# Performance work log

Hardware: AMD Instinct MI355X
Metric: run time of the kernel (lower is better)

Reference implementation:

```python
import jax, jax.numpy as jnp
import numpy as np

R = 32       # voxel_resolution
GROUPS = 8   # GroupNorm groups
EPS = 1e-5


def setup_inputs() -> dict:
    key = jax.random.key(0)
    ks = jax.random.split(key, 8)
    B, N, Cin, Cout = 4, 16384, 64, 128
    coords = jax.random.uniform(ks[0], (B, N, 3), dtype=jnp.float32)
    features = jax.random.normal(ks[1], (B, Cin, N), dtype=jnp.float32) * 0.5
    s1 = 1.0 / np.sqrt(Cin * 27)
    s2 = 1.0 / np.sqrt(Cout * 27)
    sm = 1.0 / np.sqrt(Cin)
    return {
        "coords": coords,
        "features": features,
        "conv1_w": jax.random.normal(ks[2], (Cout, Cin, 3, 3, 3), dtype=jnp.float32) * s1,
        "conv1_b": jnp.zeros((Cout,), jnp.float32),
        "gn1_g": jnp.ones((Cout,), jnp.float32),
        "gn1_b": jnp.zeros((Cout,), jnp.float32),
        "conv2_w": jax.random.normal(ks[3], (Cout, Cout, 3, 3, 3), dtype=jnp.float32) * s2,
        "conv2_b": jnp.zeros((Cout,), jnp.float32),
        "gn2_g": jnp.ones((Cout,), jnp.float32),
        "gn2_b": jnp.zeros((Cout,), jnp.float32),
        "mlp_w": jax.random.normal(ks[4], (Cout, Cin), dtype=jnp.float32) * sm,
        "mlp_b": jnp.zeros((Cout,), jnp.float32),
        "gnp_g": jnp.ones((Cout,), jnp.float32),
        "gnp_b": jnp.zeros((Cout,), jnp.float32),
    }


def _group_norm(x, gamma, beta, axes):
    # x: [B, C, ...]; normalize within channel groups over `axes` of the
    # grouped view [B, G, C//G, ...]. axes=(2,) => per-location GN (matches
    # nn.GroupNorm applied to per-voxel feature rows [Nvox, C]).
    B, C = x.shape[0], x.shape[1]
    xr = x.reshape(B, GROUPS, C // GROUPS, *x.shape[2:])
    mu = xr.mean(axis=axes, keepdims=True)
    var = ((xr - mu) ** 2).mean(axis=axes, keepdims=True)
    xn = ((xr - mu) * jax.lax.rsqrt(var + EPS)).reshape(x.shape)
    shp = (1, C) + (1,) * (x.ndim - 2)
    return xn * gamma.reshape(shp) + beta.reshape(shp)


def _conv3(x, w, b):
    y = jax.lax.conv_general_dilated(
        x, w, (1, 1, 1), 'SAME',
        dimension_numbers=('NCDHW', 'OIDHW', 'NCDHW'))
    return y + b.reshape(1, -1, 1, 1, 1)


def reference(coords, features, conv1_w, conv1_b, gn1_g, gn1_b,
              conv2_w, conv2_b, gn2_g, gn2_b, mlp_w, mlp_b, gnp_g, gnp_b):
    B, Cin, N = features.shape
    Cout = conv1_w.shape[0]

    # ---- voxelize: average-scatter point features into [B,Cin,R,R,R] ----
    c = coords * R                               # voxel-unit coords in [0,R)
    lo = jnp.floor(c)
    idx = jnp.clip(lo.astype(jnp.int32), 0, R - 1)   # [B,N,3]
    bidx = jnp.arange(B, dtype=jnp.int32)[:, None]
    flat = ((bidx * R + idx[..., 0]) * R + idx[..., 1]) * R + idx[..., 2]
    seg = flat.reshape(-1)                       # [B*N]
    fT = features.transpose(0, 2, 1).reshape(B * N, Cin)
    sums = jax.ops.segment_sum(fT, seg, num_segments=B * R * R * R)
    cnt = jax.ops.segment_sum(jnp.ones((B * N,), fT.dtype), seg,
                              num_segments=B * R * R * R)
    grid = (sums / jnp.maximum(cnt, 1.0)[:, None]).reshape(
        B, R, R, R, Cin).transpose(0, 4, 1, 2, 3)

    # ---- voxel branch: conv -> GN -> SiLU -> (dropout=id) -> conv -> GN -> SiLU
    h = jax.nn.silu(_group_norm(_conv3(grid, conv1_w, conv1_b), gn1_g, gn1_b, (2,)))
    h = jax.nn.silu(_group_norm(_conv3(h, conv2_w, conv2_b), gn2_g, gn2_b, (2,)))

    # ---- trilinear devoxelize: gather-interpolate back to points ----
    frac = c - lo                                # [B,N,3]
    hi = jnp.clip(idx + 1, 0, R - 1)
    gridf = h.transpose(0, 2, 3, 4, 1).reshape(B, R * R * R, Cout)
    barange = jnp.arange(B)[:, None]
    out = jnp.zeros((B, N, Cout), h.dtype)
    for dx in (0, 1):
        wx = frac[..., 0] if dx else 1.0 - frac[..., 0]
        ix = hi[..., 0] if dx else idx[..., 0]
        for dy in (0, 1):
            wy = frac[..., 1] if dy else 1.0 - frac[..., 1]
            iy = hi[..., 1] if dy else idx[..., 1]
            for dz in (0, 1):
                wz = frac[..., 2] if dz else 1.0 - frac[..., 2]
                iz = hi[..., 2] if dz else idx[..., 2]
                fi = (ix * R + iy) * R + iz       # [B,N]
                vals = gridf[barange, fi]         # [B,N,Cout]
                out = out + (wx * wy * wz)[..., None] * vals
    vox_pts = out.transpose(0, 2, 1)              # [B,Cout,N]

    # ---- point branch: SharedMLP = 1x1 conv + GroupNorm + SiLU ----
    pf = jnp.einsum('oi,bin->bon', mlp_w, features) + mlp_b[None, :, None]
    pf = jax.nn.silu(_group_norm(pf, gnp_g, gnp_b, (2, 3)))

    return pf + vox_pts
```

## Files before the change

### kernel.cpp

```cpp
#include <hip/hip_runtime.h>

typedef unsigned short u16;
typedef __attribute__((ext_vector_type(8))) short s16x8;
typedef __attribute__((ext_vector_type(4))) float f32x4;

#define R3 32768
#define NPTS 16384

__device__ __forceinline__ float b2f(u16 u) {
  union { unsigned int i; float f; } v; v.i = ((unsigned int)u) << 16; return v.f;
}
__device__ __forceinline__ u16 f2b(float f) {
  union { float f; unsigned int i; } v; v.f = f;
  unsigned int x = v.i;
  return (u16)((x + 0x7fffu + ((x >> 16) & 1u)) >> 16);
}
__device__ __forceinline__ void split2(float x, u16& h, u16& l) {
  h = f2b(x); l = f2b(x - b2f(h));
}
__device__ __forceinline__ float silu(float x) {
  return x / (1.f + __expf(-x));
}

__global__ void convert_weights(const float* __restrict__ w1, const float* __restrict__ w2,
                                const float* __restrict__ wm,
                                u16* __restrict__ Wh1, u16* __restrict__ Wl1,
                                u16* __restrict__ Wh2, u16* __restrict__ Wl2,
                                u16* __restrict__ Whm, u16* __restrict__ Wlm) {
  int e = blockIdx.x * 256 + threadIdx.x;
  if (e < 27 * 128 * 64) {
    int t = e / (128 * 64), co = (e / 64) % 128, ci = e % 64;
    split2(w1[(co * 64 + ci) * 27 + t], Wh1[e], Wl1[e]);
  }
  if (e < 27 * 128 * 128) {
    int t = e / (128 * 128), co = (e / 128) % 128, ci = e % 128;
    split2(w2[(co * 128 + ci) * 27 + t], Wh2[e], Wl2[e]);
  }
  if (e < 128 * 64) split2(wm[e], Whm[e], Wlm[e]);
}

__global__ void __launch_bounds__(256)
scatter_feats(const float* __restrict__ coords, const float* __restrict__ features,
              float* __restrict__ Gsum, float* __restrict__ Gcnt) {
  __shared__ float trans[64][65];
  __shared__ int vox[64];
  const int tid = threadIdx.x;
  const int bi = blockIdx.x >> 8;
  const int n0 = (blockIdx.x & 255) << 6;
  if (tid < 64) {
    const float* cp = coords + ((size_t)bi * NPTS + n0 + tid) * 3;
    int ix = min(max((int)floorf(cp[0] * 32.f), 0), 31);
    int iy = min(max((int)floorf(cp[1] * 32.f), 0), 31);
    int iz = min(max((int)floorf(cp[2] * 32.f), 0), 31);
    vox[tid] = (ix * 32 + iy) * 32 + iz;
  }
  for (int e = tid; e < 4096; e += 256) {
    int ci = e >> 6, nn = e & 63;
    trans[nn][ci] = features[((size_t)bi * 64 + ci) * NPTS + n0 + nn];
  }
  __syncthreads();
  const int wave = tid >> 6, lane = tid & 63;
  for (int pi = 0; pi < 16; ++pi) {
    int nn = wave * 16 + pi;
    int v = vox[nn];
    atomicAdd(&Gsum[((size_t)bi * R3 + v) * 64 + lane], trans[nn][lane]);
    if (lane == 0) atomicAdd(&Gcnt[bi * R3 + v], 1.f);
  }
}

__global__ void __launch_bounds__(256)
finalize_grid(const float* __restrict__ Gsum, const float* __restrict__ Gcnt,
              u16* __restrict__ X1) {
  size_t g = (size_t)blockIdx.x * 256 + threadIdx.x;
  float c = fmaxf(Gcnt[g >> 4], 1.f);
  float4 s = ((const float4*)Gsum)[g];
  unsigned h0 = f2b(s.x / c), h1 = f2b(s.y / c), h2 = f2b(s.z / c), h3 = f2b(s.w / c);
  uint2 o; o.x = h0 | (h1 << 16); o.y = h2 | (h3 << 16);
  *(uint2*)(X1 + g * 4) = o;
}

template<int CIN>
__global__ void __launch_bounds__(128, 2)
conv_mfma_w2(const u16* __restrict__ X, const u16* __restrict__ Wh, const u16* __restrict__ Wl,
             const float* __restrict__ bias, const float* __restrict__ gamma,
             const float* __restrict__ beta, u16* __restrict__ Yb) {
  constexpr int CINP = CIN + 8;
  constexpr int ROWS = 136;
  constexpr int KS = CIN / 32;
  constexpr int CH8 = CIN / 8;
  constexpr int XBYTES = ROWS * CINP * 2;
  constexpr int OBYTES = 128 * 136 * 2;
  constexpr int LBYTES = (XBYTES > OBYTES) ? XBYTES : OBYTES;
  __shared__ __align__(16) char ldsbuf[LBYTES];
  u16* Xs = (u16*)ldsbuf;
  u16* Os = (u16*)ldsbuf;

  const int tid = threadIdx.x;
  const int wave = tid >> 6, lane = tid & 63;
  const int l15 = lane & 15, q = lane >> 4;
  const int co0 = wave * 64;

  const int bi = blockIdx.x >> 8;
  const int rem = blockIdx.x & 255;
  const int x = rem >> 3, y0 = (rem & 7) << 2;

  u16 oneb = f2b(1.0f), lidb = f2b((float)(l15 + 1));
  s16x8 vone, vlid;
#pragma unroll
  for (int e = 0; e < 8; ++e) { vone[e] = (short)oneb; vlid[e] = (short)lidb; }
  f32x4 z4 = {0.f, 0.f, 0.f, 0.f};
  f32x4 d1 = __builtin_amdgcn_mfma_f32_16x16x32_bf16(vlid, vone, z4, 0, 0, 0);
  f32x4 d2 = __builtin_amdgcn_mfma_f32_16x16x32_bf16(vone, vlid, z4, 0, 0, 0);
  int mdec[4], ndec[4];
#pragma unroll
  for (int r = 0; r < 4; ++r) {
    mdec[r] = (int)(d1[r] * 0.03125f + 0.5f) - 1;
    ndec[r] = (int)(d2[r] * 0.03125f + 0.5f) - 1;
  }

  f32x4 acc[4][8];
#pragma unroll
  for (int a = 0; a < 4; ++a)
#pragma unroll
    for (int b = 0; b < 8; ++b) acc[a][b] = (f32x4){0.f, 0.f, 0.f, 0.f};

  for (int g = 0; g < 9; ++g) {
    __syncthreads();
    const int dx = g / 3 - 1, dy = g % 3 - 1;
    const int xs = x + dx;
    for (int c = tid; c < ROWS * CH8; c += 128) {
      int rr = c / CH8, k = (c % CH8) * 8;
      uint4 val; val.x = val.y = val.z = val.w = 0u;
      int vy = rr / 34;
      int zz = rr - vy * 34 - 1;
      int ys = y0 + vy + dy;
      if (xs >= 0 && xs < 32 && ys >= 0 && ys < 32 && zz >= 0 && zz < 32)
        val = *(const uint4*)(X + ((size_t)bi * R3 + (size_t)((xs * 32 + ys) * 32 + zz)) * CIN + k);
      *(uint4*)(&Xs[rr * CINP + k]) = val;
    }
    __syncthreads();
    for (int dz = 0; dz < 3; ++dz) {
      const int t = g * 3 + dz;
#pragma unroll
      for (int kb = 0; kb < KS; ++kb) {
        const int ko = kb * 32 + q * 8;
        s16x8 ah[4], al[4], bb[8];
#pragma unroll
        for (int ct = 0; ct < 4; ++ct) {
          size_t wo = ((size_t)(t * 128 + co0 + ct * 16 + l15)) * CIN + ko;
          ah[ct] = *(const s16x8*)(Wh + wo);
          al[ct] = *(const s16x8*)(Wl + wo);
        }
#pragma unroll
        for (int vt = 0; vt < 8; ++vt)
          bb[vt] = *(const s16x8*)(
              &Xs[((vt >> 1) * 34 + (vt & 1) * 16 + l15 + dz) * CINP + ko]);
#pragma unroll
        for (int ct = 0; ct < 4; ++ct)
#pragma unroll
          for (int vt = 0; vt < 8; ++vt) {
            acc[ct][vt] = __builtin_amdgcn_mfma_f32_16x16x32_bf16(
                ah[ct], bb[vt], acc[ct][vt], 0, 0, 0);
            acc[ct][vt] = __builtin_amdgcn_mfma_f32_16x16x32_bf16(
                al[ct], bb[vt], acc[ct][vt], 0, 0, 0);
          }
      }
    }
  }

  __syncthreads();
#pragma unroll
  for (int ct = 0; ct < 4; ++ct) {
    float bi4[4], g4[4], be4[4];
#pragma unroll
    for (int r = 0; r < 4; ++r) {
      int coL = co0 + ct * 16 + mdec[r];
      bi4[r] = bias[coL]; g4[r] = gamma[coL]; be4[r] = beta[coL];
    }
#pragma unroll
    for (int vt = 0; vt < 8; ++vt) {
      float v[4];
#pragma unroll
      for (int r = 0; r < 4; ++r) v[r] = acc[ct][vt][r] + bi4[r];
      float s = v[0] + v[1] + v[2] + v[3];
      s += __shfl_xor(s, 16); s += __shfl_xor(s, 32);
      float mu = s * 0.0625f;
      float qv = 0.f;
#pragma unroll
      for (int r = 0; r < 4; ++r) { float d = v[r] - mu; qv = fmaf(d, d, qv); }
      qv += __shfl_xor(qv, 16); qv += __shfl_xor(qv, 32);
      float rs = rsqrtf(qv * 0.0625f + 1e-5f);
      int vox = vt * 16 + l15;
#pragma unroll
      for (int r = 0; r < 4; ++r) {
        float xn = (v[r] - mu) * rs * g4[r] + be4[r];
        Os[vox * 136 + co0 + ct * 16 + mdec[r]] = f2b(silu(xn));
      }
    }
  }
  __syncthreads();
  for (int e = tid; e < 2048; e += 128) {
    int vox = e >> 4, c8 = (e & 15) * 8;
    int yl = vox >> 5, z = vox & 31;
    size_t row = (size_t)bi * R3 + (size_t)((x * 32 + y0 + yl) * 32 + z);
    *(uint4*)(Yb + row * 128 + c8) = *(const uint4*)(&Os[vox * 136 + c8]);
  }
}

__global__ void __launch_bounds__(256)
mlp_mfma(const float* __restrict__ features, const u16* __restrict__ Whm,
         const u16* __restrict__ Wlm, const float* __restrict__ mb,
         u16* __restrict__ pf, float* __restrict__ stats) {
  constexpr int XBYTES = 64 * 72 * 2;
  constexpr int SBYTES = 4 * 64 * 33 * 4;
  __shared__ __align__(16) char ldsbuf[(XBYTES > SBYTES) ? XBYTES : SBYTES];
  u16* Xs = (u16*)ldsbuf;
  float* ldsW = (float*)ldsbuf;

  const int tid = threadIdx.x;
  const int wave = tid >> 6, lane = tid & 63;
  const int l15 = lane & 15, q = lane >> 4;
  const int cobase = wave * 32;
  const int bi = blockIdx.x >> 8;
  const int n0 = (blockIdx.x & 255) << 6;

  u16 oneb = f2b(1.0f), lidb = f2b((float)(l15 + 1));
  s16x8 vone, vlid;
#pragma unroll
  for (int e = 0; e < 8; ++e) { vone[e] = (short)oneb; vlid[e] = (short)lidb; }
  f32x4 z4 = {0.f, 0.f, 0.f, 0.f};
  f32x4 d1 = __builtin_amdgcn_mfma_f32_16x16x32_bf16(vlid, vone, z4, 0, 0, 0);
  f32x4 d2 = __builtin_amdgcn_mfma_f32_16x16x32_bf16(vone, vlid, z4, 0, 0, 0);
  int mdec[4], ndec[4];
#pragma unroll
  for (int r = 0; r < 4; ++r) {
    mdec[r] = (int)(d1[r] * 0.03125f + 0.5f) - 1;
    ndec[r] = (int)(d2[r] * 0.03125f + 0.5f) - 1;
  }

  for (int e = tid; e < 4096; e += 256) {
    int ci = e >> 6, nn = e & 63;
    Xs[nn * 72 + ci] = f2b(features[((size_t)bi * 64 + ci) * NPTS + n0 + nn]);
  }
  __syncthreads();

  f32x4 acc[2][4];
#pragma unroll
  for (int a = 0; a < 2; ++a)
#pragma unroll
    for (int b = 0; b < 4; ++b) acc[a][b] = (f32x4){0.f, 0.f, 0.f, 0.f};

#pragma unroll
  for (int kb = 0; kb < 2; ++kb) {
    const int ko = kb * 32 + q * 8;
    s16x8 ah[2], al[2], bb[4];
#pragma unroll
    for (int ct = 0; ct < 2; ++ct) {
      size_t wo = ((size_t)(cobase + ct * 16 + l15)) * 64 + ko;
      ah[ct] = *(const s16x8*)(Whm + wo);
      al[ct] = *(const s16x8*)(Wlm + wo);
    }
#pragma unroll
    for (int vt = 0; vt < 4; ++vt)
      bb[vt] = *(const s16x8*)(&Xs[(vt * 16 + l15) * 72 + ko]);
#pragma unroll
    for (int ct = 0; ct < 2; ++ct)
#pragma unroll
      for (int vt = 0; vt < 4; ++vt) {
        acc[ct][vt] = __builtin_amdgcn_mfma_f32_16x16x32_bf16(ah[ct], bb[vt], acc[ct][vt], 0, 0, 0);
        acc[ct][vt] = __builtin_amdgcn_mfma_f32_16x16x32_bf16(al[ct], bb[vt], acc[ct][vt], 0, 0, 0);
      }
  }

  __syncthreads();
#pragma unroll
  for (int ct = 0; ct < 2; ++ct)
#pragma unroll
    for (int vt = 0; vt < 4; ++vt)
#pragma unroll
      for (int r = 0; r < 4; ++r)
        ldsW[(wave * 64 + vt * 16 + ndec[r]) * 33 + ct * 16 + mdec[r]] = acc[ct][vt][r];
  __syncthreads();

  float v[32];
  float s0 = 0.f, q0 = 0.f, s1 = 0.f, q1 = 0.f;
#pragma unroll
  for (int j = 0; j < 32; ++j) {
    v[j] = ldsW[(wave * 64 + lane) * 33 + j] + mb[cobase + j];
    if (j < 16) { s0 += v[j]; q0 = fmaf(v[j], v[j], q0); }
    else        { s1 += v[j]; q1 = fmaf(v[j], v[j], q1); }
  }
  u16 outv[32];
#pragma unroll
  for (int j = 0; j < 32; ++j) outv[j] = f2b(v[j]);
  u16* yp = pf + ((size_t)bi * NPTS + n0 + lane) * 128 + cobase;
#pragma unroll
  for (int k = 0; k < 4; ++k) *(uint4*)(yp + 8 * k) = *(uint4*)(outv + 8 * k);

#pragma unroll
  for (int off = 32; off > 0; off >>= 1) {
    s0 += __shfl_xor(s0, off); q0 += __shfl_xor(q0, off);
    s1 += __shfl_xor(s1, off); q1 += __shfl_xor(q1, off);
  }
  if (lane == 0) {
    atomicAdd(&stats[(bi * 8 + 2 * wave + 0) * 2 + 0], s0);
    atomicAdd(&stats[(bi * 8 + 2 * wave + 0) * 2 + 1], q0);
    atomicAdd(&stats[(bi * 8 + 2 * wave + 1) * 2 + 0], s1);
    atomicAdd(&stats[(bi * 8 + 2 * wave + 1) * 2 + 1], q1);
  }
}

__global__ void __launch_bounds__(256)
final_fuse(const float* __restrict__ coords, const u16* __restrict__ H,
           const u16* __restrict__ pf, const float* __restrict__ stats,
           const float* __restrict__ gg, const float* __restrict__ gb,
           float* __restrict__ out) {
  __shared__ float trans[64][130];
  const int tid = threadIdx.x;
  const int wave = tid >> 6, lane = tid & 63;
  const int bi = blockIdx.x >> 8;
  const int p0 = (blockIdx.x & 255) << 6;
  const int co = lane * 2;
  const int grp = co >> 4;
  const float cntInv = 1.f / (16.f * 16384.f);
  float S  = stats[(bi * 8 + grp) * 2 + 0];
  float SS = stats[(bi * 8 + grp) * 2 + 1];
  float mu = S * cntInv;
  float var = SS * cntInv - mu * mu;
  float rs = rsqrtf(var + 1e-5f);
  float g0 = gg[co], g1 = gg[co + 1], b0 = gb[co], b1 = gb[co + 1];

  for (int pi = 0; pi < 16; ++pi) {
    int pl = wave * 16 + pi;
    int p = p0 + pl;
    const float* cp = coords + ((size_t)bi * NPTS + p) * 3;
    float cx = cp[0] * 32.f, cy = cp[1] * 32.f, cz = cp[2] * 32.f;
    float fx = floorf(cx), fy = floorf(cy), fz = floorf(cz);
    int ix = min(max((int)fx, 0), 31);
    int iy = min(max((int)fy, 0), 31);
    int iz = min(max((int)fz, 0), 31);
    float rx = cx - fx, ry = cy - fy, rz = cz - fz;
    int hx = min(ix + 1, 31), hy = min(iy + 1, 31), hz = min(iz + 1, 31);
    float a0 = 0.f, a1 = 0.f;
#pragma unroll
    for (int k = 0; k < 8; ++k) {
      int xb = k >> 2, yb = (k >> 1) & 1, zb = k & 1;
      float w = (xb ? rx : 1.f - rx) * (yb ? ry : 1.f - ry) * (zb ? rz : 1.f - rz);
      int vi = ((xb ? hx : ix) * 32 + (yb ? hy : iy)) * 32 + (zb ? hz : iz);
      unsigned hv = *(const unsigned*)(H + ((size_t)bi * R3 + vi) * 128 + co);
      a0 += w * b2f((u16)(hv & 0xffff));
      a1 += w * b2f((u16)(hv >> 16));
    }
    unsigned pv = *(const unsigned*)(pf + ((size_t)bi * NPTS + p) * 128 + co);
    float q0 = (b2f((u16)(pv & 0xffff)) - mu) * rs * g0 + b0;
    float q1 = (b2f((u16)(pv >> 16)) - mu) * rs * g1 + b1;
    trans[pl][co]     = silu(q0) + a0;
    trans[pl][co + 1] = silu(q1) + a1;
  }
  __syncthreads();
  for (int e = tid; e < 8192; e += 256) {
    int c = e >> 6, pp = e & 63;
    out[((size_t)bi * 128 + c) * NPTS + p0 + pp] = trans[pp][c];
  }
}

extern "C" void kernel_launch(void* const* d_in, const int* in_sizes, int n_in,
                              void* d_out, int out_size, void* d_ws, size_t ws_size,
                              hipStream_t stream) {
  const float* coords   = (const float*)d_in[0];
  const float* features = (const float*)d_in[1];
  const float* conv1_w  = (const float*)d_in[2];
  const float* conv1_b  = (const float*)d_in[3];
  const float* gn1_g    = (const float*)d_in[4];
  const float* gn1_b    = (const float*)d_in[5];
  const float* conv2_w  = (const float*)d_in[6];
  const float* conv2_b  = (const float*)d_in[7];
  const float* gn2_g    = (const float*)d_in[8];
  const float* gn2_b    = (const float*)d_in[9];
  const float* mlp_w    = (const float*)d_in[10];
  const float* mlp_b    = (const float*)d_in[11];
  const float* gnp_g    = (const float*)d_in[12];
  const float* gnp_b    = (const float*)d_in[13];

  char* ws = (char*)d_ws;
  float* Gsum = (float*)(ws + 0);
  u16*   H    = (u16*)(ws + 0);
  u16*   X1   = (u16*)(ws + 33554432);
  u16*   X2   = (u16*)(ws + 50331648);
  float* Gcnt = (float*)(ws + 83886080);
  float* stats = (float*)(ws + 84410368);
  u16*   pf   = (u16*)(ws + 84676608);
  u16*   Wh1  = (u16*)(ws + 101453824);
  u16*   Wl1  = (u16*)(ws + 101896192);
  u16*   Wh2  = (u16*)(ws + 102338560);
  u16*   Wl2  = (u16*)(ws + 103223296);
  u16*   Whm  = (u16*)(ws + 104108032);
  u16*   Wlm  = (u16*)(ws + 104124416);

  hipMemsetAsync(ws, 0, 33554432, stream);
  hipMemsetAsync(ws + 83886080, 0, 524288 + 4096, stream);

  convert_weights<<<(27 * 128 * 128 + 255) / 256, 256, 0, stream>>>(
      conv1_w, conv2_w, mlp_w, Wh1, Wl1, Wh2, Wl2, Whm, Wlm);
  scatter_feats<<<1024, 256, 0, stream>>>(coords, features, Gsum, Gcnt);
  finalize_grid<<<8192, 256, 0, stream>>>(Gsum, Gcnt, X1);
  conv_mfma_w2<64><<<1024, 128, 0, stream>>>(
      X1, Wh1, Wl1, conv1_b, gn1_g, gn1_b, X2);
  mlp_mfma<<<1024, 256, 0, stream>>>(features, Whm, Wlm, mlp_b, pf, stats);
  conv_mfma_w2<128><<<1024, 128, 0, stream>>>(
      X2, Wh2, Wl2, conv2_b, gn2_g, gn2_b, H);
  final_fuse<<<1024, 256, 0, stream>>>(coords, H, pf, stats, gnp_g, gnp_b,
                                       (float*)d_out);
}
```

Before: 673.0 us.

## Restructure 3D conv to 32x32 MFMA tiles with 4 waves and x-slab staging

The conv kernel now uses 32x32x16 bf16 MFMA instead of 16x16x32 and runs 4 waves per block instead of 2. Waves split output channels in halves and voxel rows in pairs. The LDS tile now holds a 6x34 y/z slab per x offset, so only 3 staging passes and barrier pairs are needed instead of 9, and the dy shifts are taken by indexing inside LDS. The GroupNorm epilogue is rewritten for the 32x32 accumulator layout, with two groups per tile. In exchange the kernel uses more LDS per block, makes more weight loads per MFMA, and drops the occupancy hint from launch bounds.

```diff
diff --git a/kernel.cpp b/kernel.cpp
--- a/kernel.cpp
+++ b/kernel.cpp
@@ -3,6 +3,7 @@
 typedef unsigned short u16;
 typedef __attribute__((ext_vector_type(8))) short s16x8;
 typedef __attribute__((ext_vector_type(4))) float f32x4;
+typedef __attribute__((ext_vector_type(16))) float f32x16;
 
 #define R3 32768
 #define NPTS 16384
@@ -80,14 +81,15 @@
 }
 
 template<int CIN>
-__global__ void __launch_bounds__(128, 2)
-conv_mfma_w2(const u16* __restrict__ X, const u16* __restrict__ Wh, const u16* __restrict__ Wl,
-             const float* __restrict__ bias, const float* __restrict__ gamma,
-             const float* __restrict__ beta, u16* __restrict__ Yb) {
+__global__ void __launch_bounds__(256)
+conv_mfma_s32(const u16* __restrict__ X, const u16* __restrict__ Wh, const u16* __restrict__ Wl,
+              const float* __restrict__ bias, const float* __restrict__ gamma,
+              const float* __restrict__ beta, u16* __restrict__ Yb) {
   constexpr int CINP = CIN + 8;
-  constexpr int ROWS = 136;
-  constexpr int KS = CIN / 32;
+  constexpr int ROWS = 204;
   constexpr int CH8 = CIN / 8;
+  constexpr int NCH = ROWS * CH8;
+  constexpr int NSI = CIN / 16;
   constexpr int XBYTES = ROWS * CINP * 2;
   constexpr int OBYTES = 128 * 136 * 2;
   constexpr int LBYTES = (XBYTES > OBYTES) ? XBYTES : OBYTES;
@@ -97,109 +99,124 @@
 
   const int tid = threadIdx.x;
   const int wave = tid >> 6, lane = tid & 63;
-  const int l15 = lane & 15, q = lane >> 4;
-  const int co0 = wave * 64;
+  const int l31 = lane & 31, kh = lane >> 5;
+  const int cohalf = wave & 1, vh = wave >> 1;
+  const int co0 = cohalf * 64;
 
   const int bi = blockIdx.x >> 8;
   const int rem = blockIdx.x & 255;
   const int x = rem >> 3, y0 = (rem & 7) << 2;
 
-  u16 oneb = f2b(1.0f), lidb = f2b((float)(l15 + 1));
+  u16 oneb = f2b(1.0f), lidb = f2b((float)(l31 + 1));
   s16x8 vone, vlid;
 #pragma unroll
   for (int e = 0; e < 8; ++e) { vone[e] = (short)oneb; vlid[e] = (short)lidb; }
-  f32x4 z4 = {0.f, 0.f, 0.f, 0.f};
-  f32x4 d1 = __builtin_amdgcn_mfma_f32_16x16x32_bf16(vlid, vone, z4, 0, 0, 0);
-  f32x4 d2 = __builtin_amdgcn_mfma_f32_16x16x32_bf16(vone, vlid, z4, 0, 0, 0);
-  int mdec[4], ndec[4];
-#pragma unroll
-  for (int r = 0; r < 4; ++r) {
-    mdec[r] = (int)(d1[r] * 0.03125f + 0.5f) - 1;
-    ndec[r] = (int)(d2[r] * 0.03125f + 0.5f) - 1;
-  }
-
-  f32x4 acc[4][8];
-#pragma unroll
-  for (int a = 0; a < 4; ++a)
-#pragma unroll
-    for (int b = 0; b < 8; ++b) acc[a][b] = (f32x4){0.f, 0.f, 0.f, 0.f};
-
-  for (int g = 0; g < 9; ++g) {
+  f32x16 z16;
+#pragma unroll
+  for (int r = 0; r < 16; ++r) z16[r] = 0.f;
+  f32x16 d1 = __builtin_amdgcn_mfma_f32_32x32x16_bf16(vlid, vone, z16, 0, 0, 0);
+  int mdec[16];
+#pragma unroll
+  for (int r = 0; r < 16; ++r)
+    mdec[r] = (int)(d1[r] * 0.0625f + 0.5f) - 1;
+
+  f32x16 acc[2][2];
+#pragma unroll
+  for (int a = 0; a < 2; ++a)
+#pragma unroll
+    for (int b = 0; b < 2; ++b)
+#pragma unroll
+      for (int r = 0; r < 16; ++r) acc[a][b][r] = 0.f;
+
+  for (int dxs = 0; dxs < 3; ++dxs) {
     __syncthreads();
-    const int dx = g / 3 - 1, dy = g % 3 - 1;
-    const int xs = x + dx;
-    for (int c = tid; c < ROWS * CH8; c += 128) {
+    const int xs = x + dxs - 1;
+    for (int c = tid; c < NCH; c += 256) {
       int rr = c / CH8, k = (c % CH8) * 8;
       uint4 val; val.x = val.y = val.z = val.w = 0u;
-      int vy = rr / 34;
-      int zz = rr - vy * 34 - 1;
-      int ys = y0 + vy + dy;
+      int jy = rr / 34;
+      int pz = rr - jy * 34;
+      int ys = y0 + jy - 1, zz = pz - 1;
       if (xs >= 0 && xs < 32 && ys >= 0 && ys < 32 && zz >= 0 && zz < 32)
         val = *(const uint4*)(X + ((size_t)bi * R3 + (size_t)((xs * 32 + ys) * 32 + zz)) * CIN + k);
       *(uint4*)(&Xs[rr * CINP + k]) = val;
     }
     __syncthreads();
-    for (int dz = 0; dz < 3; ++dz) {
-      const int t = g * 3 + dz;
-#pragma unroll
-      for (int kb = 0; kb < KS; ++kb) {
-        const int ko = kb * 32 + q * 8;
-        s16x8 ah[4], al[4], bb[8];
-#pragma unroll
-        for (int ct = 0; ct < 4; ++ct) {
-          size_t wo = ((size_t)(t * 128 + co0 + ct * 16 + l15)) * CIN + ko;
-          ah[ct] = *(const s16x8*)(Wh + wo);
-          al[ct] = *(const s16x8*)(Wl + wo);
+    for (int dy = 0; dy < 3; ++dy) {
+      const int tb = dxs * 9 + dy * 3;
+#pragma unroll
+      for (int dz = 0; dz < 3; ++dz) {
+        const int t = tb + dz;
+#pragma unroll
+        for (int si = 0; si < NSI; ++si) {
+          const int ko = si * 16 + kh * 8;
+          s16x8 ah[2], al[2], bb[2];
+#pragma unroll
+          for (int ct = 0; ct < 2; ++ct) {
+            size_t wo = ((size_t)(t * 128 + co0 + ct * 32 + l31)) * CIN + ko;
+            ah[ct] = *(const s16x8*)(Wh + wo);
+            al[ct] = *(const s16x8*)(Wl + wo);
+          }
+#pragma unroll
+          for (int vt = 0; vt < 2; ++vt)
+            bb[vt] = *(const s16x8*)(
+                &Xs[((dy + vh * 2 + vt) * 34 + l31 + dz) * CINP + ko]);
+#pragma unroll
+          for (int ct = 0; ct < 2; ++ct)
+#pragma unroll
+            for (int vt = 0; vt < 2; ++vt) {
+              acc[ct][vt] = __builtin_amdgcn_mfma_f32_32x32x16_bf16(
+                  ah[ct], bb[vt], acc[ct][vt], 0, 0, 0);
+              acc[ct][vt] = __builtin_amdgcn_mfma_f32_32x32x16_bf16(
+                  al[ct], bb[vt], acc[ct][vt], 0, 0, 0);
+            }
         }
-#pragma unroll
-        for (int vt = 0; vt < 8; ++vt)
-          bb[vt] = *(const s16x8*)(
-              &Xs[((vt >> 1) * 34 + (vt & 1) * 16 + l15 + dz) * CINP + ko]);
-#pragma unroll
-        for (int ct = 0; ct < 4; ++ct)
-#pragma unroll
-          for (int vt = 0; vt < 8; ++vt) {
-            acc[ct][vt] = __builtin_amdgcn_mfma_f32_16x16x32_bf16(
-                ah[ct], bb[vt], acc[ct][vt], 0, 0, 0);
-            acc[ct][vt] = __builtin_amdgcn_mfma_f32_16x16x32_bf16(
-                al[ct], bb[vt], acc[ct][vt], 0, 0, 0);
-          }
       }
     }
   }
 
   __syncthreads();
 #pragma unroll
-  for (int ct = 0; ct < 4; ++ct) {
-    float bi4[4], g4[4], be4[4];
-#pragma unroll
-    for (int r = 0; r < 4; ++r) {
-      int coL = co0 + ct * 16 + mdec[r];
-      bi4[r] = bias[coL]; g4[r] = gamma[coL]; be4[r] = beta[coL];
-    }
-#pragma unroll
-    for (int vt = 0; vt < 8; ++vt) {
-      float v[4];
-#pragma unroll
-      for (int r = 0; r < 4; ++r) v[r] = acc[ct][vt][r] + bi4[r];
-      float s = v[0] + v[1] + v[2] + v[3];
-      s += __shfl_xor(s, 16); s += __shfl_xor(s, 32);
-      float mu = s * 0.0625f;
-      float qv = 0.f;
-#pragma unroll
-      for (int r = 0; r < 4; ++r) { float d = v[r] - mu; qv = fmaf(d, d, qv); }
-      qv += __shfl_xor(qv, 16); qv += __shfl_xor(qv, 32);
-      float rs = rsqrtf(qv * 0.0625f + 1e-5f);
-      int vox = vt * 16 + l15;
-#pragma unroll
-      for (int r = 0; r < 4; ++r) {
-        float xn = (v[r] - mu) * rs * g4[r] + be4[r];
-        Os[vox * 136 + co0 + ct * 16 + mdec[r]] = f2b(silu(xn));
+  for (int ct = 0; ct < 2; ++ct) {
+    float bi16[16], g16[16], be16[16];
+#pragma unroll
+    for (int r = 0; r < 16; ++r) {
+      int coL = co0 + ct * 32 + mdec[r];
+      bi16[r] = bias[coL]; g16[r] = gamma[coL]; be16[r] = beta[coL];
+    }
+#pragma unroll
+    for (int vt = 0; vt < 2; ++vt) {
+      float vv[16];
+      float s0 = 0.f, s1 = 0.f;
+#pragma unroll
+      for (int r = 0; r < 16; ++r) {
+        vv[r] = acc[ct][vt][r] + bi16[r];
+        if (mdec[r] < 16) s0 += vv[r]; else s1 += vv[r];
       }
-    }
-  }
-  __syncthreads();
-  for (int e = tid; e < 2048; e += 128) {
+      s0 += __shfl_xor(s0, 32); s1 += __shfl_xor(s1, 32);
+      float mu0 = s0 * 0.0625f, mu1 = s1 * 0.0625f;
+      float q0 = 0.f, q1 = 0.f;
+#pragma unroll
+      for (int r = 0; r < 16; ++r) {
+        float mu = (mdec[r] < 16) ? mu0 : mu1;
+        float d = vv[r] - mu;
+        if (mdec[r] < 16) q0 = fmaf(d, d, q0); else q1 = fmaf(d, d, q1);
+      }
+      q0 += __shfl_xor(q0, 32); q1 += __shfl_xor(q1, 32);
+      float rs0 = rsqrtf(q0 * 0.0625f + 1e-5f);
+      float rs1 = rsqrtf(q1 * 0.0625f + 1e-5f);
+      int vox = (vh * 2 + vt) * 32 + l31;
+#pragma unroll
+      for (int r = 0; r < 16; ++r) {
+        float mu = (mdec[r] < 16) ? mu0 : mu1;
+        float rs = (mdec[r] < 16) ? rs0 : rs1;
+        float xn = (vv[r] - mu) * rs * g16[r] + be16[r];
+        Os[vox * 136 + co0 + ct * 32 + mdec[r]] = f2b(silu(xn));
+      }
+    }
+  }
+  __syncthreads();
+  for (int e = tid; e < 2048; e += 256) {
     int vox = e >> 4, c8 = (e & 15) * 8;
     int yl = vox >> 5, z = vox & 31;
     size_t row = (size_t)bi * R3 + (size_t)((x * 32 + y0 + yl) * 32 + z);
@@ -404,10 +421,10 @@
       conv1_w, conv2_w, mlp_w, Wh1, Wl1, Wh2, Wl2, Whm, Wlm);
   scatter_feats<<<1024, 256, 0, stream>>>(coords, features, Gsum, Gcnt);
   finalize_grid<<<8192, 256, 0, stream>>>(Gsum, Gcnt, X1);
-  conv_mfma_w2<64><<<1024, 128, 0, stream>>>(
+  conv_mfma_s32<64><<<1024, 256, 0, stream>>>(
       X1, Wh1, Wl1, conv1_b, gn1_g, gn1_b, X2);
   mlp_mfma<<<1024, 256, 0, stream>>>(features, Whm, Wlm, mlp_b, pf, stats);
-  conv_mfma_w2<128><<<1024, 128, 0, stream>>>(
+  conv_mfma_s32<128><<<1024, 256, 0, stream>>>(
       X2, Wh2, Wl2, conv2_b, gn2_g, gn2_b, H);
   final_fuse<<<1024, 256, 0, stream>>>(coords, H, pf, stats, gnp_g, gnp_b,
                                        (float*)d_out);
```

Result: slower. 1.015 ms (+50.8%).
